# Kernel optimization log

Measured on AMD Instinct MI355X. Metric: run time of the kernel, lower is better.

The kernel has to match this reference:

```python
import jax, jax.numpy as jnp
import numpy as np

H = 4096          # hidden_size
I = 2048          # moe_intermediate_size * n_shared_experts
SWIGLU_LIMIT = 10.0
QMAX = 127.0


def _quantize_weight(w):
    # per-output-channel symmetric int8 quantization of a float weight [out, in]
    s = jnp.maximum(jnp.max(jnp.abs(w), axis=1) / QMAX, 1e-8)      # [out]
    q = jnp.clip(jnp.round(w / s[:, None]), -QMAX, QMAX)           # int8-valued
    return q.astype(jnp.float32), s.astype(jnp.float32)


def setup_inputs() -> dict:
    key = jax.random.key(0)
    ks = jax.random.split(key, 4)
    x = jax.random.normal(ks[0], (2, 4096, H), dtype=jnp.float32)
    w_gate, s_wgate = _quantize_weight(jax.random.normal(ks[1], (I, H)) * 0.02)
    w_up, s_wup = _quantize_weight(jax.random.normal(ks[2], (I, H)) * 0.02)
    w_down, s_wdown = _quantize_weight(jax.random.normal(ks[3], (H, I)) * 0.02)
    inv_gate = jnp.ones((H,), jnp.float32)
    inv_up = jnp.ones((H,), jnp.float32)
    inv_inter = jnp.ones((I,), jnp.float32)
    return {"x": x, "w_gate": w_gate, "s_wgate": s_wgate, "w_up": w_up,
            "s_wup": s_wup, "w_down": w_down, "s_wdown": s_wdown,
            "inv_gate": inv_gate, "inv_up": inv_up, "inv_inter": inv_inter}


def _dynamic_quant(x, inv_smooth):
    # per-token symmetric int8 dynamic quant with smoothing scale
    xs = x.astype(jnp.float32) * inv_smooth                        # [T, D]
    scale = jnp.maximum(jnp.max(jnp.abs(xs), axis=-1, keepdims=True) / QMAX, 1e-8)
    q = jnp.clip(jnp.round(xs / scale), -QMAX, QMAX)
    return q, scale


def _quant_gemm(q, x_scale, w_q, w_scale):
    acc = q @ w_q.T                                                # fp32 accumulate
    return acc * x_scale * w_scale[None, :]


def reference(x, w_gate, s_wgate, w_up, s_wup, w_down, s_wdown,
              inv_gate, inv_up, inv_inter):
    orig_shape = x.shape
    x_flat = x.reshape(-1, H).astype(jnp.bfloat16)                 # [T, H]
    qg, sg = _dynamic_quant(x_flat, inv_gate)
    qu, su = _dynamic_quant(x_flat, inv_up)
    gate_out = _quant_gemm(qg, sg, w_gate, s_wgate)                # [T, I]
    up_out = _quant_gemm(qu, su, w_up, s_wup)                      # [T, I]
    inter = jax.nn.silu(gate_out) * up_out
    inter = jnp.clip(inter, -SWIGLU_LIMIT, SWIGLU_LIMIT).astype(jnp.bfloat16)
    qi, si = _dynamic_quant(inter, inv_inter)
    out = _quant_gemm(qi, si, w_down, s_wdown)                     # [T, H]
    return out.reshape(orig_shape)
```

## Files before the change

kernel.cpp:

```cpp
#include <hip/hip_runtime.h>
#include <hip/hip_bf16.h>


typedef __attribute__((ext_vector_type(4))) int i32x4;

__device__ __forceinline__ void async16(void* lds, const void* g) {
  __builtin_amdgcn_global_load_lds(
      (const __attribute__((address_space(1))) void*)g,
      (__attribute__((address_space(3))) void*)lds, 16, 0, 0);
}

__device__ __forceinline__ i32x4 mfma_i8(i32x4 a, i32x4 b, i32x4 c) {
  return __builtin_amdgcn_mfma_i32_16x16x64_i8(a, b, c, 0, 0, 0);
}

__device__ __forceinline__ float bf16_rne_f(float f) {
  unsigned u = __float_as_uint(f);
  u += 0x7fffu + ((u >> 16) & 1u);
  return __uint_as_float(u & 0xffff0000u);
}

__device__ __forceinline__ unsigned short bf16_bits(float f) {
  unsigned u = __float_as_uint(f);
  u += 0x7fffu + ((u >> 16) & 1u);
  return (unsigned short)(u >> 16);
}

__device__ __forceinline__ float bf16_to_f(unsigned short h) {
  return __uint_as_float(((unsigned)h) << 16);
}

__global__ void wconv_kernel(const float* __restrict__ w,
                             signed char* __restrict__ wq, int n) {
  int i = (blockIdx.x * 256 + threadIdx.x) * 4;
  if (i >= n) return;
  float4 f = *(const float4*)(w + i);
  signed char c[4] __attribute__((aligned(4)));
  c[0] = (signed char)(int)rintf(f.x);
  c[1] = (signed char)(int)rintf(f.y);
  c[2] = (signed char)(int)rintf(f.z);
  c[3] = (signed char)(int)rintf(f.w);
  *(int*)(wq + i) = *(const int*)c;
}

__global__ __launch_bounds__(256) void quant_x_kernel(
    const float* __restrict__ x, const float* __restrict__ invg,
    const float* __restrict__ invu, signed char* __restrict__ qg,
    signed char* __restrict__ qu, float* __restrict__ sg,
    float* __restrict__ su, int H) {
  const int t = blockIdx.x, tid = threadIdx.x;
  const float* xr = x + (size_t)t * H;
  const int c0 = tid * 16;
  float xg[16], xu[16];
  float mg = 0.f, mu = 0.f;
#pragma unroll
  for (int v = 0; v < 4; ++v) {
    float4 f = *(const float4*)(xr + c0 + v * 4);
    float4 ig = *(const float4*)(invg + c0 + v * 4);
    float4 iu = *(const float4*)(invu + c0 + v * 4);
    float b0 = bf16_rne_f(f.x), b1 = bf16_rne_f(f.y);
    float b2 = bf16_rne_f(f.z), b3 = bf16_rne_f(f.w);
    xg[v * 4 + 0] = b0 * ig.x; xg[v * 4 + 1] = b1 * ig.y;
    xg[v * 4 + 2] = b2 * ig.z; xg[v * 4 + 3] = b3 * ig.w;
    xu[v * 4 + 0] = b0 * iu.x; xu[v * 4 + 1] = b1 * iu.y;
    xu[v * 4 + 2] = b2 * iu.z; xu[v * 4 + 3] = b3 * iu.w;
#pragma unroll
    for (int j = 0; j < 4; ++j) {
      mg = fmaxf(mg, fabsf(xg[v * 4 + j]));
      mu = fmaxf(mu, fabsf(xu[v * 4 + j]));
    }
  }
#pragma unroll
  for (int off = 32; off > 0; off >>= 1) {
    mg = fmaxf(mg, __shfl_xor(mg, off));
    mu = fmaxf(mu, __shfl_xor(mu, off));
  }
  __shared__ float smg[4], smu[4];
  if ((tid & 63) == 0) { smg[tid >> 6] = mg; smu[tid >> 6] = mu; }
  __syncthreads();
  mg = fmaxf(fmaxf(smg[0], smg[1]), fmaxf(smg[2], smg[3]));
  mu = fmaxf(fmaxf(smu[0], smu[1]), fmaxf(smu[2], smu[3]));
  const float scg = fmaxf(mg / 127.0f, 1e-8f);
  const float scu = fmaxf(mu / 127.0f, 1e-8f);
  signed char og[16] __attribute__((aligned(16)));
  signed char ou[16] __attribute__((aligned(16)));
#pragma unroll
  for (int j = 0; j < 16; ++j) {
    og[j] = (signed char)(int)fminf(fmaxf(rintf(xg[j] / scg), -127.f), 127.f);
    ou[j] = (signed char)(int)fminf(fmaxf(rintf(xu[j] / scu), -127.f), 127.f);
  }
  *(i32x4*)(qg + (size_t)t * H + c0) = *(const i32x4*)og;
  *(i32x4*)(qu + (size_t)t * H + c0) = *(const i32x4*)ou;
  if (tid == 0) { sg[t] = scg; su[t] = scu; }
}

__global__ __launch_bounds__(256, 2) void gemm1_kernel(
    const signed char* __restrict__ qg, const signed char* __restrict__ qu,
    const float* __restrict__ sg, const float* __restrict__ su,
    const signed char* __restrict__ wg, const signed char* __restrict__ wu,
    const float* __restrict__ swg, const float* __restrict__ swu,
    unsigned short* __restrict__ inter, int H, int I) {
  __shared__ signed char Ag[128 * 64] __attribute__((aligned(16)));
  __shared__ signed char Au[128 * 64] __attribute__((aligned(16)));
  __shared__ signed char Bg[128 * 64] __attribute__((aligned(16)));
  __shared__ signed char Bu[128 * 64] __attribute__((aligned(16)));
  const int tid = threadIdx.x;
  const int lane = tid & 63, wave = tid >> 6;
  const int row0 = blockIdx.x * 128, col0 = blockIdx.y * 128;
  const int wm = (wave & 1) * 64, wn = (wave >> 1) * 64;
  const int mrow = lane & 15, quad = lane >> 4;

  i32x4 accG[4][4], accU[4][4];
#pragma unroll
  for (int i = 0; i < 4; ++i)
#pragma unroll
    for (int j = 0; j < 4; ++j) {
      accG[i][j] = i32x4{0, 0, 0, 0};
      accU[i][j] = i32x4{0, 0, 0, 0};
    }

  for (int kk = 0; kk < H; kk += 64) {
    __syncthreads();
#pragma unroll
    for (int p = 0; p < 2; ++p) {
      const int g = p * 256 + tid;
      const int r = g >> 2, cb = (g & 3) << 4;
      const size_t ga = (size_t)(row0 + r) * H + kk + cb;
      const size_t gb = (size_t)(col0 + r) * H + kk + cb;
      async16(&Ag[g * 16], qg + ga);
      async16(&Au[g * 16], qu + ga);
      async16(&Bg[g * 16], wg + gb);
      async16(&Bu[g * 16], wu + gb);
    }
    __syncthreads();
    i32x4 aG[4], aU[4], bG[4], bU[4];
#pragma unroll
    for (int i = 0; i < 4; ++i) {
      aG[i] = *(const i32x4*)&Ag[(wm + i * 16 + mrow) * 64 + quad * 16];
      aU[i] = *(const i32x4*)&Au[(wm + i * 16 + mrow) * 64 + quad * 16];
      bG[i] = *(const i32x4*)&Bg[(wn + i * 16 + mrow) * 64 + quad * 16];
      bU[i] = *(const i32x4*)&Bu[(wn + i * 16 + mrow) * 64 + quad * 16];
    }
#pragma unroll
    for (int i = 0; i < 4; ++i)
#pragma unroll
      for (int j = 0; j < 4; ++j) {
        accG[i][j] = mfma_i8(aG[i], bG[j], accG[i][j]);
        accU[i][j] = mfma_i8(aU[i], bU[j], accU[i][j]);
      }
  }

  float swgc[4], swuc[4];
#pragma unroll
  for (int j = 0; j < 4; ++j) {
    const int c = col0 + wn + j * 16 + mrow;
    swgc[j] = swg[c];
    swuc[j] = swu[c];
  }
#pragma unroll
  for (int i = 0; i < 4; ++i) {
#pragma unroll
    for (int r = 0; r < 4; ++r) {
      const int row = row0 + wm + i * 16 + quad * 4 + r;
      const float sgr = sg[row], sur = su[row];
#pragma unroll
      for (int j = 0; j < 4; ++j) {
        const int c = col0 + wn + j * 16 + mrow;
        const float g = (float)accG[i][j][r] * sgr * swgc[j];
        const float u = (float)accU[i][j][r] * sur * swuc[j];
        const float sig = 1.f / (1.f + expf(-g));
        float v = (g * sig) * u;
        v = fminf(fmaxf(v, -10.f), 10.f);
        inter[(size_t)row * I + c] = bf16_bits(v);
      }
    }
  }
}

__global__ __launch_bounds__(256) void quant_i_kernel(
    const unsigned short* __restrict__ inter, const float* __restrict__ invi,
    signed char* __restrict__ qi, float* __restrict__ si, int I) {
  const int t = blockIdx.x, tid = threadIdx.x;
  const unsigned short* ir = inter + (size_t)t * I;
  const int c0 = tid * 8;
  uint4 pk = *(const uint4*)(ir + c0);
  float4 i0 = *(const float4*)(invi + c0);
  float4 i1 = *(const float4*)(invi + c0 + 4);
  float xs[8];
  xs[0] = bf16_to_f(pk.x & 0xffffu) * i0.x;
  xs[1] = bf16_to_f(pk.x >> 16) * i0.y;
  xs[2] = bf16_to_f(pk.y & 0xffffu) * i0.z;
  xs[3] = bf16_to_f(pk.y >> 16) * i0.w;
  xs[4] = bf16_to_f(pk.z & 0xffffu) * i1.x;
  xs[5] = bf16_to_f(pk.z >> 16) * i1.y;
  xs[6] = bf16_to_f(pk.w & 0xffffu) * i1.z;
  xs[7] = bf16_to_f(pk.w >> 16) * i1.w;
  float m = 0.f;
#pragma unroll
  for (int j = 0; j < 8; ++j) m = fmaxf(m, fabsf(xs[j]));
#pragma unroll
  for (int off = 32; off > 0; off >>= 1) m = fmaxf(m, __shfl_xor(m, off));
  __shared__ float sm[4];
  if ((tid & 63) == 0) sm[tid >> 6] = m;
  __syncthreads();
  m = fmaxf(fmaxf(sm[0], sm[1]), fmaxf(sm[2], sm[3]));
  const float s = fmaxf(m / 127.0f, 1e-8f);
  signed char o[8] __attribute__((aligned(8)));
#pragma unroll
  for (int j = 0; j < 8; ++j)
    o[j] = (signed char)(int)fminf(fmaxf(rintf(xs[j] / s), -127.f), 127.f);
  *(unsigned long long*)(qi + (size_t)t * I + c0) = *(const unsigned long long*)o;
  if (tid == 0) si[t] = s;
}

__global__ __launch_bounds__(256, 2) void gemm2_kernel(
    const signed char* __restrict__ qi, const float* __restrict__ si,
    const signed char* __restrict__ wd, const float* __restrict__ swd,
    float* __restrict__ out, int H, int I) {
  __shared__ signed char As[128 * 64] __attribute__((aligned(16)));
  __shared__ signed char Bs[128 * 64] __attribute__((aligned(16)));
  const int tid = threadIdx.x;
  const int lane = tid & 63, wave = tid >> 6;
  const int row0 = blockIdx.x * 128, col0 = blockIdx.y * 128;
  const int wm = (wave & 1) * 64, wn = (wave >> 1) * 64;
  const int mrow = lane & 15, quad = lane >> 4;

  i32x4 acc[4][4];
#pragma unroll
  for (int i = 0; i < 4; ++i)
#pragma unroll
    for (int j = 0; j < 4; ++j) acc[i][j] = i32x4{0, 0, 0, 0};

  for (int kk = 0; kk < I; kk += 64) {
    __syncthreads();
#pragma unroll
    for (int p = 0; p < 2; ++p) {
      const int g = p * 256 + tid;
      const int r = g >> 2, cb = (g & 3) << 4;
      async16(&As[g * 16], qi + (size_t)(row0 + r) * I + kk + cb);
      async16(&Bs[g * 16], wd + (size_t)(col0 + r) * I + kk + cb);
    }
    __syncthreads();
    i32x4 a[4], b[4];
#pragma unroll
    for (int i = 0; i < 4; ++i) {
      a[i] = *(const i32x4*)&As[(wm + i * 16 + mrow) * 64 + quad * 16];
      b[i] = *(const i32x4*)&Bs[(wn + i * 16 + mrow) * 64 + quad * 16];
    }
#pragma unroll
    for (int i = 0; i < 4; ++i)
#pragma unroll
      for (int j = 0; j < 4; ++j) acc[i][j] = mfma_i8(a[i], b[j], acc[i][j]);
  }

  float swc[4];
#pragma unroll
  for (int j = 0; j < 4; ++j) swc[j] = swd[col0 + wn + j * 16 + mrow];
#pragma unroll
  for (int i = 0; i < 4; ++i) {
#pragma unroll
    for (int r = 0; r < 4; ++r) {
      const int row = row0 + wm + i * 16 + quad * 4 + r;
      const float sir = si[row];
#pragma unroll
      for (int j = 0; j < 4; ++j) {
        const int c = col0 + wn + j * 16 + mrow;
        out[(size_t)row * H + c] = (float)acc[i][j][r] * sir * swc[j];
      }
    }
  }
}

extern "C" void kernel_launch(void* const* d_in, const int* in_sizes, int n_in,
                              void* d_out, int out_size, void* d_ws,
                              size_t ws_size, hipStream_t stream) {
  const float* x = (const float*)d_in[0];
  const float* w_gate = (const float*)d_in[1];
  const float* s_wgate = (const float*)d_in[2];
  const float* w_up = (const float*)d_in[3];
  const float* s_wup = (const float*)d_in[4];
  const float* w_down = (const float*)d_in[5];
  const float* s_wdown = (const float*)d_in[6];
  const float* inv_gate = (const float*)d_in[7];
  const float* inv_up = (const float*)d_in[8];
  const float* inv_inter = (const float*)d_in[9];
  float* out = (float*)d_out;

  const int H = in_sizes[6];
  const int I = in_sizes[2];
  const int T = in_sizes[0] / H;

  char* ws = (char*)d_ws;
  size_t off = 0;
  signed char* wqg = (signed char*)(ws + off); off += (size_t)I * H;
  signed char* wqu = (signed char*)(ws + off); off += (size_t)I * H;
  signed char* wqd = (signed char*)(ws + off); off += (size_t)H * I;
  signed char* qg  = (signed char*)(ws + off); off += (size_t)T * H;
  signed char* qu  = (signed char*)(ws + off); off += (size_t)T * H;
  unsigned short* inter = (unsigned short*)(ws + off); off += (size_t)T * I * 2;
  float* sg = (float*)(ws + off); off += (size_t)T * 4;
  float* su = (float*)(ws + off); off += (size_t)T * 4;
  float* si = (float*)(ws + off); off += (size_t)T * 4;
  signed char* qi = qg;

  const int nW = I * H;
  wconv_kernel<<<nW / 1024, 256, 0, stream>>>(w_gate, wqg, nW);
  wconv_kernel<<<nW / 1024, 256, 0, stream>>>(w_up, wqu, nW);
  wconv_kernel<<<nW / 1024, 256, 0, stream>>>(w_down, wqd, nW);

  quant_x_kernel<<<T, 256, 0, stream>>>(x, inv_gate, inv_up, qg, qu, sg, su, H);

  dim3 g1(T / 128, I / 128);
  gemm1_kernel<<<g1, 256, 0, stream>>>(qg, qu, sg, su, wqg, wqu, s_wgate,
                                       s_wup, inter, H, I);

  quant_i_kernel<<<T, 256, 0, stream>>>(inter, inv_inter, qi, si, I);

  dim3 g2(T / 128, H / 128);
  gemm2_kernel<<<g2, 256, 0, stream>>>(qi, si, wqd, s_wdown, out, H, I);
}
```

Measured before the change: 606.7 us.

## Use 32x32 int8 MFMA with swizzled LDS, fused weight conversion, reciprocal quant

```diff
diff --git a/kernel.cpp b/kernel.cpp
--- a/kernel.cpp
+++ b/kernel.cpp
@@ -3,6 +3,7 @@
 
 
 typedef __attribute__((ext_vector_type(4))) int i32x4;
+typedef __attribute__((ext_vector_type(16))) int i32x16;
 
 __device__ __forceinline__ void async16(void* lds, const void* g) {
   __builtin_amdgcn_global_load_lds(
@@ -10,8 +11,8 @@
       (__attribute__((address_space(3))) void*)lds, 16, 0, 0);
 }
 
-__device__ __forceinline__ i32x4 mfma_i8(i32x4 a, i32x4 b, i32x4 c) {
-  return __builtin_amdgcn_mfma_i32_16x16x64_i8(a, b, c, 0, 0, 0);
+__device__ __forceinline__ i32x16 mfma32(i32x4 a, i32x4 b, i32x16 c) {
+  return __builtin_amdgcn_mfma_i32_32x32x32_i8(a, b, c, 0, 0, 0);
 }
 
 __device__ __forceinline__ float bf16_rne_f(float f) {
@@ -19,19 +20,23 @@
   u += 0x7fffu + ((u >> 16) & 1u);
   return __uint_as_float(u & 0xffff0000u);
 }
-
 __device__ __forceinline__ unsigned short bf16_bits(float f) {
   unsigned u = __float_as_uint(f);
   u += 0x7fffu + ((u >> 16) & 1u);
   return (unsigned short)(u >> 16);
 }
-
 __device__ __forceinline__ float bf16_to_f(unsigned short h) {
   return __uint_as_float(((unsigned)h) << 16);
 }
 
-__global__ void wconv_kernel(const float* __restrict__ w,
-                             signed char* __restrict__ wq, int n) {
+__global__ void wconv3_kernel(const float* __restrict__ w0,
+                              const float* __restrict__ w1,
+                              const float* __restrict__ w2,
+                              signed char* __restrict__ q0,
+                              signed char* __restrict__ q1,
+                              signed char* __restrict__ q2, int n) {
+  const float* w = (blockIdx.y == 0) ? w0 : (blockIdx.y == 1) ? w1 : w2;
+  signed char* q = (blockIdx.y == 0) ? q0 : (blockIdx.y == 1) ? q1 : q2;
   int i = (blockIdx.x * 256 + threadIdx.x) * 4;
   if (i >= n) return;
   float4 f = *(const float4*)(w + i);
@@ -40,7 +45,7 @@
   c[1] = (signed char)(int)rintf(f.y);
   c[2] = (signed char)(int)rintf(f.z);
   c[3] = (signed char)(int)rintf(f.w);
-  *(int*)(wq + i) = *(const int*)c;
+  *(int*)(q + i) = *(const int*)c;
 }
 
 __global__ __launch_bounds__(256) void quant_x_kernel(
@@ -82,12 +87,13 @@
   mu = fmaxf(fmaxf(smu[0], smu[1]), fmaxf(smu[2], smu[3]));
   const float scg = fmaxf(mg / 127.0f, 1e-8f);
   const float scu = fmaxf(mu / 127.0f, 1e-8f);
+  const float rg = 1.0f / scg, ru = 1.0f / scu;
   signed char og[16] __attribute__((aligned(16)));
   signed char ou[16] __attribute__((aligned(16)));
 #pragma unroll
   for (int j = 0; j < 16; ++j) {
-    og[j] = (signed char)(int)fminf(fmaxf(rintf(xg[j] / scg), -127.f), 127.f);
-    ou[j] = (signed char)(int)fminf(fmaxf(rintf(xu[j] / scu), -127.f), 127.f);
+    og[j] = (signed char)(int)fminf(fmaxf(rintf(xg[j] * rg), -127.f), 127.f);
+    ou[j] = (signed char)(int)fminf(fmaxf(rintf(xu[j] * ru), -127.f), 127.f);
   }
   *(i32x4*)(qg + (size_t)t * H + c0) = *(const i32x4*)og;
   *(i32x4*)(qu + (size_t)t * H + c0) = *(const i32x4*)ou;
@@ -106,17 +112,17 @@
   __shared__ signed char Bu[128 * 64] __attribute__((aligned(16)));
   const int tid = threadIdx.x;
   const int lane = tid & 63, wave = tid >> 6;
-  const int row0 = blockIdx.x * 128, col0 = blockIdx.y * 128;
+  const int col0 = blockIdx.x * 128, row0 = blockIdx.y * 128;
   const int wm = (wave & 1) * 64, wn = (wave >> 1) * 64;
-  const int mrow = lane & 15, quad = lane >> 4;
-
-  i32x4 accG[4][4], accU[4][4];
-#pragma unroll
-  for (int i = 0; i < 4; ++i)
-#pragma unroll
-    for (int j = 0; j < 4; ++j) {
-      accG[i][j] = i32x4{0, 0, 0, 0};
-      accU[i][j] = i32x4{0, 0, 0, 0};
+  const int m = lane & 31, h = lane >> 5;
+
+  i32x16 accG[2][2], accU[2][2];
+#pragma unroll
+  for (int i = 0; i < 2; ++i)
+#pragma unroll
+    for (int j = 0; j < 2; ++j) {
+      accG[i][j] = (i32x16)(0);
+      accU[i][j] = (i32x16)(0);
     }
 
   for (int kk = 0; kk < H; kk += 64) {
@@ -124,51 +130,59 @@
 #pragma unroll
     for (int p = 0; p < 2; ++p) {
       const int g = p * 256 + tid;
-      const int r = g >> 2, cb = (g & 3) << 4;
-      const size_t ga = (size_t)(row0 + r) * H + kk + cb;
-      const size_t gb = (size_t)(col0 + r) * H + kk + cb;
+      const int r = g >> 2;
+      const int cg = ((g & 3) - r) & 3;
+      const size_t ga = (size_t)(row0 + r) * H + kk + cg * 16;
+      const size_t gb = (size_t)(col0 + r) * H + kk + cg * 16;
       async16(&Ag[g * 16], qg + ga);
       async16(&Au[g * 16], qu + ga);
       async16(&Bg[g * 16], wg + gb);
       async16(&Bu[g * 16], wu + gb);
     }
     __syncthreads();
-    i32x4 aG[4], aU[4], bG[4], bU[4];
-#pragma unroll
-    for (int i = 0; i < 4; ++i) {
-      aG[i] = *(const i32x4*)&Ag[(wm + i * 16 + mrow) * 64 + quad * 16];
-      aU[i] = *(const i32x4*)&Au[(wm + i * 16 + mrow) * 64 + quad * 16];
-      bG[i] = *(const i32x4*)&Bg[(wn + i * 16 + mrow) * 64 + quad * 16];
-      bU[i] = *(const i32x4*)&Bu[(wn + i * 16 + mrow) * 64 + quad * 16];
-    }
-#pragma unroll
-    for (int i = 0; i < 4; ++i)
-#pragma unroll
-      for (int j = 0; j < 4; ++j) {
-        accG[i][j] = mfma_i8(aG[i], bG[j], accG[i][j]);
-        accU[i][j] = mfma_i8(aU[i], bU[j], accU[i][j]);
+#pragma unroll
+    for (int s = 0; s < 2; ++s) {
+      i32x4 aG[2], aU[2], bG[2], bU[2];
+#pragma unroll
+      for (int i = 0; i < 2; ++i) {
+        const int ra = wm + i * 32 + m;
+        const int ca = ((s * 2 + h + ra) & 3) * 16;
+        aG[i] = *(const i32x4*)&Ag[ra * 64 + ca];
+        aU[i] = *(const i32x4*)&Au[ra * 64 + ca];
+        const int rb = wn + i * 32 + m;
+        const int cb = ((s * 2 + h + rb) & 3) * 16;
+        bG[i] = *(const i32x4*)&Bg[rb * 64 + cb];
+        bU[i] = *(const i32x4*)&Bu[rb * 64 + cb];
       }
-  }
-
-  float swgc[4], swuc[4];
-#pragma unroll
-  for (int j = 0; j < 4; ++j) {
-    const int c = col0 + wn + j * 16 + mrow;
+#pragma unroll
+      for (int i = 0; i < 2; ++i)
+#pragma unroll
+        for (int j = 0; j < 2; ++j) {
+          accG[i][j] = mfma32(aG[i], bG[j], accG[i][j]);
+          accU[i][j] = mfma32(aU[i], bU[j], accU[i][j]);
+        }
+    }
+  }
+
+  float swgc[2], swuc[2];
+#pragma unroll
+  for (int j = 0; j < 2; ++j) {
+    const int c = col0 + wn + j * 32 + m;
     swgc[j] = swg[c];
     swuc[j] = swu[c];
   }
 #pragma unroll
-  for (int i = 0; i < 4; ++i) {
-#pragma unroll
-    for (int r = 0; r < 4; ++r) {
-      const int row = row0 + wm + i * 16 + quad * 4 + r;
+  for (int i = 0; i < 2; ++i) {
+#pragma unroll
+    for (int reg = 0; reg < 16; ++reg) {
+      const int row = row0 + wm + i * 32 + (reg & 3) + 8 * (reg >> 2) + 4 * h;
       const float sgr = sg[row], sur = su[row];
 #pragma unroll
-      for (int j = 0; j < 4; ++j) {
-        const int c = col0 + wn + j * 16 + mrow;
-        const float g = (float)accG[i][j][r] * sgr * swgc[j];
-        const float u = (float)accU[i][j][r] * sur * swuc[j];
-        const float sig = 1.f / (1.f + expf(-g));
+      for (int j = 0; j < 2; ++j) {
+        const int c = col0 + wn + j * 32 + m;
+        const float g = (float)accG[i][j][reg] * sgr * swgc[j];
+        const float u = (float)accU[i][j][reg] * sur * swuc[j];
+        const float sig = 1.f / (1.f + __expf(-g));
         float v = (g * sig) * u;
         v = fminf(fmaxf(v, -10.f), 10.f);
         inter[(size_t)row * I + c] = bf16_bits(v);
@@ -205,10 +219,11 @@
   __syncthreads();
   m = fmaxf(fmaxf(sm[0], sm[1]), fmaxf(sm[2], sm[3]));
   const float s = fmaxf(m / 127.0f, 1e-8f);
+  const float rs = 1.0f / s;
   signed char o[8] __attribute__((aligned(8)));
 #pragma unroll
   for (int j = 0; j < 8; ++j)
-    o[j] = (signed char)(int)fminf(fmaxf(rintf(xs[j] / s), -127.f), 127.f);
+    o[j] = (signed char)(int)fminf(fmaxf(rintf(xs[j] * rs), -127.f), 127.f);
   *(unsigned long long*)(qi + (size_t)t * I + c0) = *(const unsigned long long*)o;
   if (tid == 0) si[t] = s;
 }
@@ -221,51 +236,59 @@
   __shared__ signed char Bs[128 * 64] __attribute__((aligned(16)));
   const int tid = threadIdx.x;
   const int lane = tid & 63, wave = tid >> 6;
-  const int row0 = blockIdx.x * 128, col0 = blockIdx.y * 128;
+  const int col0 = blockIdx.x * 128, row0 = blockIdx.y * 128;
   const int wm = (wave & 1) * 64, wn = (wave >> 1) * 64;
-  const int mrow = lane & 15, quad = lane >> 4;
-
-  i32x4 acc[4][4];
-#pragma unroll
-  for (int i = 0; i < 4; ++i)
-#pragma unroll
-    for (int j = 0; j < 4; ++j) acc[i][j] = i32x4{0, 0, 0, 0};
+  const int m = lane & 31, h = lane >> 5;
+
+  i32x16 acc[2][2];
+#pragma unroll
+  for (int i = 0; i < 2; ++i)
+#pragma unroll
+    for (int j = 0; j < 2; ++j) acc[i][j] = (i32x16)(0);
 
   for (int kk = 0; kk < I; kk += 64) {
     __syncthreads();
 #pragma unroll
     for (int p = 0; p < 2; ++p) {
       const int g = p * 256 + tid;
-      const int r = g >> 2, cb = (g & 3) << 4;
-      async16(&As[g * 16], qi + (size_t)(row0 + r) * I + kk + cb);
-      async16(&Bs[g * 16], wd + (size_t)(col0 + r) * I + kk + cb);
+      const int r = g >> 2;
+      const int cg = ((g & 3) - r) & 3;
+      async16(&As[g * 16], qi + (size_t)(row0 + r) * I + kk + cg * 16);
+      async16(&Bs[g * 16], wd + (size_t)(col0 + r) * I + kk + cg * 16);
     }
     __syncthreads();
-    i32x4 a[4], b[4];
-#pragma unroll
-    for (int i = 0; i < 4; ++i) {
-      a[i] = *(const i32x4*)&As[(wm + i * 16 + mrow) * 64 + quad * 16];
-      b[i] = *(const i32x4*)&Bs[(wn + i * 16 + mrow) * 64 + quad * 16];
-    }
-#pragma unroll
-    for (int i = 0; i < 4; ++i)
-#pragma unroll
-      for (int j = 0; j < 4; ++j) acc[i][j] = mfma_i8(a[i], b[j], acc[i][j]);
-  }
-
-  float swc[4];
-#pragma unroll
-  for (int j = 0; j < 4; ++j) swc[j] = swd[col0 + wn + j * 16 + mrow];
-#pragma unroll
-  for (int i = 0; i < 4; ++i) {
-#pragma unroll
-    for (int r = 0; r < 4; ++r) {
-      const int row = row0 + wm + i * 16 + quad * 4 + r;
+#pragma unroll
+    for (int s = 0; s < 2; ++s) {
+      i32x4 a[2], b[2];
+#pragma unroll
+      for (int i = 0; i < 2; ++i) {
+        const int ra = wm + i * 32 + m;
+        const int ca = ((s * 2 + h + ra) & 3) * 16;
+        a[i] = *(const i32x4*)&As[ra * 64 + ca];
+        const int rb = wn + i * 32 + m;
+        const int cb = ((s * 2 + h + rb) & 3) * 16;
+        b[i] = *(const i32x4*)&Bs[rb * 64 + cb];
+      }
+#pragma unroll
+      for (int i = 0; i < 2; ++i)
+#pragma unroll
+        for (int j = 0; j < 2; ++j) acc[i][j] = mfma32(a[i], b[j], acc[i][j]);
+    }
+  }
+
+  float swc[2];
+#pragma unroll
+  for (int j = 0; j < 2; ++j) swc[j] = swd[col0 + wn + j * 32 + m];
+#pragma unroll
+  for (int i = 0; i < 2; ++i) {
+#pragma unroll
+    for (int reg = 0; reg < 16; ++reg) {
+      const int row = row0 + wm + i * 32 + (reg & 3) + 8 * (reg >> 2) + 4 * h;
       const float sir = si[row];
 #pragma unroll
-      for (int j = 0; j < 4; ++j) {
-        const int c = col0 + wn + j * 16 + mrow;
-        out[(size_t)row * H + c] = (float)acc[i][j][r] * sir * swc[j];
+      for (int j = 0; j < 2; ++j) {
+        const int c = col0 + wn + j * 32 + m;
+        out[(size_t)row * H + c] = (float)acc[i][j][reg] * sir * swc[j];
       }
     }
   }
@@ -304,18 +327,17 @@
   signed char* qi = qg;
 
   const int nW = I * H;
-  wconv_kernel<<<nW / 1024, 256, 0, stream>>>(w_gate, wqg, nW);
-  wconv_kernel<<<nW / 1024, 256, 0, stream>>>(w_up, wqu, nW);
-  wconv_kernel<<<nW / 1024, 256, 0, stream>>>(w_down, wqd, nW);
+  dim3 gw(nW / 1024, 3);
+  wconv3_kernel<<<gw, 256, 0, stream>>>(w_gate, w_up, w_down, wqg, wqu, wqd, nW);
 
   quant_x_kernel<<<T, 256, 0, stream>>>(x, inv_gate, inv_up, qg, qu, sg, su, H);
 
-  dim3 g1(T / 128, I / 128);
+  dim3 g1(I / 128, T / 128);
   gemm1_kernel<<<g1, 256, 0, stream>>>(qg, qu, sg, su, wqg, wqu, s_wgate,
                                        s_wup, inter, H, I);
 
   quant_i_kernel<<<T, 256, 0, stream>>>(inter, inv_inter, qi, si, I);
 
-  dim3 g2(T / 128, H / 128);
+  dim3 g2(H / 128, T / 128);
   gemm2_kernel<<<g2, 256, 0, stream>>>(qi, si, wqd, s_wdown, out, H, I);
 }
```

New measurement: 608.2 us. Within noise of the previous version (+0.2%).
